# Kernel optimization log

Hardware: AMD Instinct MI355X
Metric: run time of the kernel (lower is better)

## Reference

```python
import jax, jax.numpy as jnp
import numpy as np

B, N, DIM = 4, 16384, 256
H, D, G = 8, 64, 32  # heads, dim_head, slice_num; inner = H*D = 512


def setup_inputs() -> dict:
    key = jax.random.key(0)
    ks = jax.random.split(key, 12)
    inner = H * D
    s = lambda fan_in: 1.0 / np.sqrt(fan_in)
    inp = {
        "x": jax.random.normal(ks[0], (B, N, DIM), jnp.float32),
        # weights stored (in, out) so forward is x @ W + b
        "Wfx": jax.random.uniform(ks[1], (DIM, inner), jnp.float32, -s(DIM), s(DIM)),
        "bfx": jnp.zeros((inner,), jnp.float32),
        "Wx": jax.random.uniform(ks[2], (DIM, inner), jnp.float32, -s(DIM), s(DIM)),
        "bx": jnp.zeros((inner,), jnp.float32),
        "Wslice": jnp.linalg.qr(jax.random.normal(ks[3], (D, G), jnp.float32))[0],  # orthogonal init
        "bslice": jnp.zeros((G,), jnp.float32),
        "temperature": jnp.full((1, H, 1, 1), 0.5, jnp.float32),
        "Wq": jax.random.uniform(ks[4], (D, D), jnp.float32, -s(D), s(D)),
        "Wk": jax.random.uniform(ks[5], (D, D), jnp.float32, -s(D), s(D)),
        "Wv": jax.random.uniform(ks[6], (D, D), jnp.float32, -s(D), s(D)),
        "Wout": jax.random.uniform(ks[7], (inner, DIM), jnp.float32, -s(inner), s(inner)),
        "bout": jnp.zeros((DIM,), jnp.float32),
    }
    return inp


def reference(x, Wfx, bfx, Wx, bx, Wslice, bslice, temperature, Wq, Wk, Wv, Wout, bout):
    b, n, _ = x.shape
    # projections -> [B, H, N, D]
    fx_mid = (x @ Wfx + bfx).reshape(b, n, H, D).transpose(0, 2, 1, 3)
    x_mid = (x @ Wx + bx).reshape(b, n, H, D).transpose(0, 2, 1, 3)
    # soft slice assignment: [B, H, N, G]
    slice_logits = (x_mid @ Wslice + bslice) / temperature
    slice_weights = jax.nn.softmax(slice_logits, axis=-1)
    slice_norm = slice_weights.sum(axis=2)  # [B, H, G]
    # soft pooling to G slice tokens: [B, H, G, D]
    slice_token = jnp.einsum("bhnd,bhng->bhgd", fx_mid, slice_weights)
    slice_token = slice_token / (slice_norm[..., None] + 1e-5)
    # tiny attention over G tokens
    q = slice_token @ Wq
    k = slice_token @ Wk
    v = slice_token @ Wv
    scores = jnp.einsum("bhgd,bhkd->bhgk", q, k) / jnp.sqrt(jnp.asarray(D, q.dtype))
    attn = jax.nn.softmax(scores, axis=-1)
    out_slice = jnp.einsum("bhgk,bhkd->bhgd", attn, v)
    # scatter back to N points: [B, H, N, D] -> [B, N, H*D]
    out_x = jnp.einsum("bhgd,bhng->bhnd", out_slice, slice_weights)
    out_x = out_x.transpose(0, 2, 1, 3).reshape(b, n, H * D)
    return out_x @ Wout + bout
```

## Files before the change

kernel.cpp:

```cpp
#include <hip/hip_runtime.h>


typedef unsigned short u16;
typedef __attribute__((ext_vector_type(8))) unsigned short ushort8v;
typedef __attribute__((ext_vector_type(4))) unsigned short ushort4v;
typedef __attribute__((ext_vector_type(8))) short short8v;
typedef __attribute__((ext_vector_type(4))) float f32x4;

constexpr int Nc = 16384;
constexpr int BNc = 65536;

__device__ inline float b2f(u16 v) {
    union { unsigned int u; float f; } t; t.u = ((unsigned int)v) << 16; return t.f;
}
__device__ inline u16 f2b(float f) {
    union { float f; unsigned int u; } t; t.f = f;
    unsigned int u = t.u;
    return (u16)((u + 0x7fffu + ((u >> 16) & 1u)) >> 16);
}

__global__ __launch_bounds__(256) void k0_fold(
    const float* __restrict__ Wx, const float* __restrict__ Wslice,
    const float* __restrict__ bx, const float* __restrict__ bslice,
    u16* __restrict__ WxsT, float* __restrict__ bxs)
{
    int blk = blockIdx.x, tid = threadIdx.x;
    int h = tid >> 5, g = tid & 31;
    if (blk < 256) {
        int k = blk;
        float acc = 0.f;
        for (int d = 0; d < 64; d++)
            acc += Wx[k * 512 + h * 64 + d] * Wslice[d * 32 + g];
        WxsT[tid * 256 + k] = f2b(acc);
    } else {
        float acc = 0.f;
        for (int d = 0; d < 64; d++)
            acc += bx[h * 64 + d] * Wslice[d * 32 + g];
        bxs[tid] = acc + bslice[g];
    }
}

__global__ __launch_bounds__(256) void kprep_wfx(const float* __restrict__ Wfx,
                                                 u16* __restrict__ WfxT)
{
    int n = blockIdx.x, k = threadIdx.x;
    WfxT[n * 256 + k] = f2b(Wfx[k * 512 + n]);
}

template <int MODE, int NT>
__global__ __launch_bounds__(256, 2) void kgemm(
    const void* __restrict__ Ap, const u16* __restrict__ Bt,
    const float* __restrict__ bias, const float* __restrict__ temp,
    void* __restrict__ O1, u16* __restrict__ O2)
{
    constexpr int Kd = 256;
    __shared__ u16 Asl[4][64][8];
    __shared__ u16 Bsl[NT * 16][4][8];
    int tid = threadIdx.x;
    int wave = tid >> 6, lane = tid & 63;
    int lm = lane & 15, quad = lane >> 4;
    int row0 = blockIdx.x * 64;
    int sm = tid >> 2, skb = tid & 3;
    const u16* BtB = Bt;
    if (MODE == 2) BtB += (size_t)(row0 >> 14) * 65536;
    f32x4 acc[NT] = {};

    for (int k0 = 0; k0 < Kd; k0 += 32) {
        if (MODE < 2) {
            const float* A32 = (const float*)Ap;
            const f32x4* src = (const f32x4*)(A32 + (size_t)(row0 + sm) * Kd + k0 + skb * 8);
            f32x4 v0 = src[0], v1 = src[1];
            ushort8v o;
#pragma unroll
            for (int j = 0; j < 4; j++) { o[j] = f2b(v0[j]); o[4 + j] = f2b(v1[j]); }
            *(ushort8v*)&Asl[skb][sm][0] = o;
        } else {
            const u16* A16 = (const u16*)Ap;
            *(ushort8v*)&Asl[skb][sm][0] =
                *(const ushort8v*)(A16 + (size_t)(row0 + sm) * Kd + k0 + skb * 8);
        }
#pragma unroll
        for (int i = 0; i < NT / 4; i++) {
            int e = i * 256 + tid;
            int sn = e >> 2, sk = e & 3;
            *(ushort8v*)&Bsl[sn][sk][0] =
                *(const ushort8v*)(BtB + (size_t)sn * Kd + k0 + sk * 8);
        }
        __syncthreads();
        short8v af = *(short8v*)&Asl[quad][wave * 16 + lm][0];
#pragma unroll
        for (int nt = 0; nt < NT; nt++) {
            short8v bf = *(short8v*)&Bsl[nt * 16 + lm][quad][0];
            acc[nt] = __builtin_amdgcn_mfma_f32_16x16x32_bf16(af, bf, acc[nt], 0, 0, 0);
        }
        __syncthreads();
    }

    if (MODE == 0) {
        u16* fxT = (u16*)O1;
        int nbase = row0 + wave * 16 + quad * 4;
#pragma unroll
        for (int nt = 0; nt < NT; nt++) {
            int c = nt * 16 + lm;
            float bv = bias[c];
            ushort4v o;
#pragma unroll
            for (int r = 0; r < 4; r++) o[r] = f2b(acc[nt][r] + bv);
            *(ushort4v*)(fxT + (size_t)c * 65536 + nbase) = o;
        }
    } else if (MODE == 1) {
        int b = row0 >> 14;
        int nlbase = (row0 & 16383) + wave * 16 + quad * 4;
        u16* swb = (u16*)O1;
#pragma unroll
        for (int h = 0; h < 8; h++) {
            float it = 1.0f / temp[h];
            float bv0 = bias[h * 32 + lm];
            float bv1 = bias[h * 32 + 16 + lm];
            ushort4v p0, p1;
#pragma unroll
            for (int r = 0; r < 4; r++) {
                float v0 = (acc[2 * h][r] + bv0) * it;
                float v1 = (acc[2 * h + 1][r] + bv1) * it;
                float m = fmaxf(v0, v1);
                m = fmaxf(m, __shfl_xor(m, 1));
                m = fmaxf(m, __shfl_xor(m, 2));
                m = fmaxf(m, __shfl_xor(m, 4));
                m = fmaxf(m, __shfl_xor(m, 8));
                float e0 = __expf(v0 - m), e1 = __expf(v1 - m);
                float s = e0 + e1;
                s += __shfl_xor(s, 1);
                s += __shfl_xor(s, 2);
                s += __shfl_xor(s, 4);
                s += __shfl_xor(s, 8);
                float rs = 1.0f / s;
                float w0 = e0 * rs, w1 = e1 * rs;
                int row = row0 + wave * 16 + quad * 4 + r;
                swb[(size_t)row * 256 + h * 32 + lm] = f2b(w0);
                swb[(size_t)row * 256 + h * 32 + 16 + lm] = f2b(w1);
                p0[r] = f2b(w0); p1[r] = f2b(w1);
            }
            size_t gbase = (size_t)((b * 8 + h) * 32);
            *(ushort4v*)(O2 + (gbase + lm) * 16384 + nlbase) = p0;
            *(ushort4v*)(O2 + (gbase + 16 + lm) * 16384 + nlbase) = p1;
        }
    } else {
        float* out = (float*)O1;
#pragma unroll
        for (int nt = 0; nt < NT; nt++) {
            int c = nt * 16 + lm;
            float bv = bias[c];
#pragma unroll
            for (int r = 0; r < 4; r++)
                out[(size_t)(row0 + wave * 16 + quad * 4 + r) * 256 + c] = acc[nt][r] + bv;
        }
    }
}

__global__ __launch_bounds__(256) void k4_token_mfma(
    const u16* __restrict__ swT, const u16* __restrict__ fxT,
    float* __restrict__ token_part, float* __restrict__ norm_part)
{
    int bh = blockIdx.x, ky = blockIdx.y;
    int b = bh >> 3, h = bh & 7;
    int tid = threadIdx.x, wave = tid >> 6, lane = tid & 63;
    int lm = lane & 15, quad = lane >> 4;
    int mt = wave & 1, dp = wave >> 1;
    const u16* Ar = swT + ((size_t)(bh * 32 + mt * 16 + lm)) * 16384 + ky * 512 + quad * 8;
    const u16* Br0 = fxT + ((size_t)(h * 64 + dp * 32 + lm)) * 65536
                     + (size_t)b * 16384 + ky * 512 + quad * 8;
    const u16* Br1 = Br0 + (size_t)16 * 65536;
    f32x4 acc0 = {}, acc1 = {};
    float nacc = 0.f;
#pragma unroll
    for (int kk = 0; kk < 16; kk++) {
        short8v af = *(const short8v*)(Ar + kk * 32);
        short8v b0 = *(const short8v*)(Br0 + kk * 32);
        short8v b1 = *(const short8v*)(Br1 + kk * 32);
        acc0 = __builtin_amdgcn_mfma_f32_16x16x32_bf16(af, b0, acc0, 0, 0, 0);
        acc1 = __builtin_amdgcn_mfma_f32_16x16x32_bf16(af, b1, acc1, 0, 0, 0);
        if (dp == 0) {
            ushort8v au = (ushort8v&)af;
#pragma unroll
            for (int j = 0; j < 8; j++) nacc += b2f(au[j]);
        }
    }
    float* tp = token_part + ((size_t)(ky * 32 + bh)) * 2048;
#pragma unroll
    for (int r = 0; r < 4; r++) {
        int g = mt * 16 + quad * 4 + r;
        tp[g * 64 + dp * 32 + lm] = acc0[r];
        tp[g * 64 + dp * 32 + 16 + lm] = acc1[r];
    }
    if (dp == 0) {
        nacc += __shfl_xor(nacc, 16);
        nacc += __shfl_xor(nacc, 32);
        if (lane < 16)
            norm_part[(ky * 32 + bh) * 32 + mt * 16 + lm] = nacc;
    }
}

__global__ __launch_bounds__(256) void k4b_reduce(
    const float* __restrict__ tp, const float* __restrict__ np,
    float* __restrict__ tl)
{
    int t = blockIdx.x * 256 + threadIdx.x;
    int bh = t >> 11, e = t & 2047, g = e >> 6;
    float ts = 0.f, ns = 0.f;
    for (int ch = 0; ch < 32; ch++) {
        ts += tp[((size_t)(ch * 32 + bh)) * 2048 + e];
        ns += np[(ch * 32 + bh) * 32 + g];
    }
    tl[t] = ts / (ns + 1e-5f);
}

__global__ __launch_bounds__(256) void k5_attn(
    const float* __restrict__ tlg,
    const float* __restrict__ Wq, const float* __restrict__ Wk, const float* __restrict__ Wv,
    float* __restrict__ out_slice)
{
    __shared__ float tl[32][64];
    __shared__ float ql[32][64], kl[32][64], vl[32][64];
    __shared__ float sl[32][33];
    int bh = blockIdx.x, tid = threadIdx.x;
    const float* tk = tlg + (size_t)bh * 2048;

#pragma unroll
    for (int j = 0; j < 8; j++) {
        int idx = j * 256 + tid;
        tl[idx >> 6][idx & 63] = tk[idx];
    }
    __syncthreads();
#pragma unroll
    for (int j = 0; j < 8; j++) {
        int idx = j * 256 + tid;
        int g = idx >> 6, d = idx & 63;
        float aq = 0.f, ak = 0.f, av = 0.f;
        for (int e = 0; e < 64; e++) {
            float t = tl[g][e];
            aq += t * Wq[e * 64 + d];
            ak += t * Wk[e * 64 + d];
            av += t * Wv[e * 64 + d];
        }
        ql[g][d] = aq; kl[g][d] = ak; vl[g][d] = av;
    }
    __syncthreads();
#pragma unroll
    for (int j = 0; j < 4; j++) {
        int idx = j * 256 + tid;
        int gq = idx >> 5, gk = idx & 31;
        float s = 0.f;
        for (int d = 0; d < 64; d++) s += ql[gq][d] * kl[gk][d];
        sl[gq][gk] = s * 0.125f;
    }
    __syncthreads();
    if (tid < 32) {
        float m = -1e30f;
        for (int k2 = 0; k2 < 32; k2++) m = fmaxf(m, sl[tid][k2]);
        float s = 0.f;
        for (int k2 = 0; k2 < 32; k2++) { float e = __expf(sl[tid][k2] - m); sl[tid][k2] = e; s += e; }
        float r = 1.0f / s;
        for (int k2 = 0; k2 < 32; k2++) sl[tid][k2] *= r;
    }
    __syncthreads();
#pragma unroll
    for (int j = 0; j < 8; j++) {
        int idx = j * 256 + tid;
        int g = idx >> 6, d = idx & 63;
        float a = 0.f;
        for (int k2 = 0; k2 < 32; k2++) a += sl[g][k2] * vl[k2][d];
        out_slice[(size_t)bh * 2048 + idx] = a;
    }
}

__global__ __launch_bounds__(256) void kZ(
    const float* __restrict__ os, const float* __restrict__ Wout,
    u16* __restrict__ ZT)
{
    int b = blockIdx.x, cb = blockIdx.y;
    int t = threadIdx.x;
    int c = cb * 16 + (t & 15), kq = t >> 4;
    for (int k = kq * 16; k < kq * 16 + 16; k++) {
        int h = k >> 5, g = k & 31;
        const float* osr = os + ((size_t)(b * 8 + h)) * 2048 + g * 64;
        float acc = 0.f;
        for (int d = 0; d < 64; d++)
            acc += osr[d] * Wout[(h * 64 + d) * 256 + c];
        ZT[(size_t)b * 65536 + c * 256 + k] = f2b(acc);
    }
}

extern "C" void kernel_launch(void* const* d_in, const int* in_sizes, int n_in,
                              void* d_out, int out_size, void* d_ws, size_t ws_size,
                              hipStream_t stream)
{
    const float* x      = (const float*)d_in[0];
    const float* Wfx    = (const float*)d_in[1];
    const float* bfx    = (const float*)d_in[2];
    const float* Wx     = (const float*)d_in[3];
    const float* bx     = (const float*)d_in[4];
    const float* Wslice = (const float*)d_in[5];
    const float* bslice = (const float*)d_in[6];
    const float* temp   = (const float*)d_in[7];
    const float* Wq     = (const float*)d_in[8];
    const float* Wk     = (const float*)d_in[9];
    const float* Wv     = (const float*)d_in[10];
    const float* Wout   = (const float*)d_in[11];
    const float* bout   = (const float*)d_in[12];

    char* ws = (char*)d_ws;
    size_t off = 0;
    auto alloc = [&](size_t bytes) {
        void* p = ws + off;
        off = (off + bytes + 255) & ~(size_t)255;
        return p;
    };
    u16*   fxT   = (u16*)  alloc((size_t)512 * BNc * 2);
    u16*   swb   = (u16*)  alloc((size_t)BNc * 256 * 2);
    u16*   swT   = (u16*)  alloc((size_t)1024 * Nc * 2);
    float* tp    = (float*)alloc((size_t)1024 * 2048 * 4);
    float* np    = (float*)alloc(32768 * 4);
    float* tl    = (float*)alloc(65536 * 4);
    float* osl   = (float*)alloc(65536 * 4);
    u16*   ZT    = (u16*)  alloc(4 * 65536 * 2);
    u16*   WfxT  = (u16*)  alloc(512 * 256 * 2);
    u16*   WxsT  = (u16*)  alloc(256 * 256 * 2);
    float* bxs   = (float*)alloc(256 * 4);

    k0_fold<<<257, 256, 0, stream>>>(Wx, Wslice, bx, bslice, WxsT, bxs);
    kprep_wfx<<<512, 256, 0, stream>>>(Wfx, WfxT);

    kgemm<0, 32><<<1024, 256, 0, stream>>>(x, WfxT, bfx, nullptr, fxT, nullptr);

    kgemm<1, 16><<<1024, 256, 0, stream>>>(x, WxsT, bxs, temp, swb, swT);

    k4_token_mfma<<<dim3(32, 32), 256, 0, stream>>>(swT, fxT, tp, np);
    k4b_reduce<<<256, 256, 0, stream>>>(tp, np, tl);
    k5_attn<<<32, 256, 0, stream>>>(tl, Wq, Wk, Wv, osl);
    kZ<<<dim3(4, 16), 256, 0, stream>>>(osl, Wout, ZT);

    kgemm<2, 16><<<1024, 256, 0, stream>>>(swb, ZT, bout, nullptr, d_out, nullptr);
}
```

Before: 383.3 us.

## Fuse partial token reduction into attention kernel and stage QKV weights in LDS

Removes the separate k4b_reduce launch and the tl buffer. The 32 chunk partials of tokens and norms are now summed inside k5_attn, which also normalizes them there. Wq/Wk/Wv are loaded once into padded shared memory instead of being read from global memory inside the inner loop. The trade-off is that the reduction now runs on only 32 blocks instead of 256, so each block reads about 256KB serially. That gives less parallelism for this memory-bound step, in exchange for one fewer launch and round trip.

```diff
diff --git a/kernel.cpp b/kernel.cpp
--- a/kernel.cpp
+++ b/kernel.cpp
@@ -200,35 +200,51 @@
     }
 }
 
-__global__ __launch_bounds__(256) void k4b_reduce(
+__global__ __launch_bounds__(256) void k5_attn(
     const float* __restrict__ tp, const float* __restrict__ np,
-    float* __restrict__ tl)
-{
-    int t = blockIdx.x * 256 + threadIdx.x;
-    int bh = t >> 11, e = t & 2047, g = e >> 6;
-    float ts = 0.f, ns = 0.f;
-    for (int ch = 0; ch < 32; ch++) {
-        ts += tp[((size_t)(ch * 32 + bh)) * 2048 + e];
-        ns += np[(ch * 32 + bh) * 32 + g];
-    }
-    tl[t] = ts / (ns + 1e-5f);
-}
-
-__global__ __launch_bounds__(256) void k5_attn(
-    const float* __restrict__ tlg,
     const float* __restrict__ Wq, const float* __restrict__ Wk, const float* __restrict__ Wv,
     float* __restrict__ out_slice)
 {
-    __shared__ float tl[32][64];
-    __shared__ float ql[32][64], kl[32][64], vl[32][64];
+    __shared__ float W[3][64][65];
+    __shared__ float tl[32][65];
+    __shared__ float ql[32][65], kl[32][65], vl[32][65];
     __shared__ float sl[32][33];
+    __shared__ float nsh[32];
     int bh = blockIdx.x, tid = threadIdx.x;
-    const float* tk = tlg + (size_t)bh * 2048;
-
+
+    {
+        const float* srcs[3] = { Wq, Wk, Wv };
+#pragma unroll
+        for (int m = 0; m < 3; m++) {
+            const f32x4* src = (const f32x4*)srcs[m];
+#pragma unroll
+            for (int i = 0; i < 4; i++) {
+                int e4 = i * 256 + tid;
+                f32x4 v = src[e4];
+                int row = e4 >> 4, col = (e4 & 15) * 4;
+#pragma unroll
+                for (int j = 0; j < 4; j++) W[m][row][col + j] = v[j];
+            }
+        }
+    }
+    if (tid < 32) {
+        float ns = 0.f;
+        for (int ch = 0; ch < 32; ch++) ns += np[(ch * 32 + bh) * 32 + tid];
+        nsh[tid] = ns + 1e-5f;
+    }
 #pragma unroll
     for (int j = 0; j < 8; j++) {
-        int idx = j * 256 + tid;
-        tl[idx >> 6][idx & 63] = tk[idx];
+        int e = j * 256 + tid;
+        float ts = 0.f;
+        for (int ch = 0; ch < 32; ch++)
+            ts += tp[((size_t)(ch * 32 + bh)) * 2048 + e];
+        tl[e >> 6][e & 63] = ts;
+    }
+    __syncthreads();
+#pragma unroll
+    for (int j = 0; j < 8; j++) {
+        int e = j * 256 + tid;
+        tl[e >> 6][e & 63] /= nsh[e >> 6];
     }
     __syncthreads();
 #pragma unroll
@@ -238,9 +254,9 @@
         float aq = 0.f, ak = 0.f, av = 0.f;
         for (int e = 0; e < 64; e++) {
             float t = tl[g][e];
-            aq += t * Wq[e * 64 + d];
-            ak += t * Wk[e * 64 + d];
-            av += t * Wv[e * 64 + d];
+            aq += t * W[0][e][d];
+            ak += t * W[1][e][d];
+            av += t * W[2][e][d];
         }
         ql[g][d] = aq; kl[g][d] = ak; vl[g][d] = av;
     }
@@ -320,7 +336,6 @@
     u16*   swT   = (u16*)  alloc((size_t)1024 * Nc * 2);
     float* tp    = (float*)alloc((size_t)1024 * 2048 * 4);
     float* np    = (float*)alloc(32768 * 4);
-    float* tl    = (float*)alloc(65536 * 4);
     float* osl   = (float*)alloc(65536 * 4);
     u16*   ZT    = (u16*)  alloc(4 * 65536 * 2);
     u16*   WfxT  = (u16*)  alloc(512 * 256 * 2);
@@ -335,8 +350,7 @@
     kgemm<1, 16><<<1024, 256, 0, stream>>>(x, WxsT, bxs, temp, swb, swT);
 
     k4_token_mfma<<<dim3(32, 32), 256, 0, stream>>>(swT, fxT, tp, np);
-    k4b_reduce<<<256, 256, 0, stream>>>(tp, np, tl);
-    k5_attn<<<32, 256, 0, stream>>>(tl, Wq, Wk, Wv, osl);
+    k5_attn<<<32, 256, 0, stream>>>(tp, np, Wq, Wk, Wv, osl);
     kZ<<<dim3(4, 16), 256, 0, stream>>>(osl, Wout, ZT);
 
     kgemm<2, 16><<<1024, 256, 0, stream>>>(swb, ZT, bout, nullptr, d_out, nullptr);
```

Measured after the change: 404.0 us. +5.4%, slower.
